# Performance work log

Hardware: AMD Instinct MI355X
Metric: run time of the kernel (lower is better)

## Reference

```python
import jax, jax.numpy as jnp
import numpy as np

B, T, NT, H, L, F, NH, R = 2, 1024, 30, 1024, 8, 2816, 16, 16
HD = H // NH
LORA_SCALE = 32.0 / 16.0  # lora_alpha / r
CLAMP = 10.0
EPS = 1e-6


def _rms(x, w):
    return x * jax.lax.rsqrt(jnp.mean(x * x, axis=-1, keepdims=True) + EPS) * w


def _rope(x):
    # x: [B,T,NH,HD] -- LLaMA rotary embedding
    half = HD // 2
    inv_freq = 1.0 / (10000.0 ** (jnp.arange(0, half, dtype=jnp.float32) / half))
    ang = jnp.arange(x.shape[1], dtype=jnp.float32)[:, None] * inv_freq  # [T,half]
    cos = jnp.concatenate([jnp.cos(ang), jnp.cos(ang)], -1)[None, :, None, :]
    sin = jnp.concatenate([jnp.sin(ang), jnp.sin(ang)], -1)[None, :, None, :]
    x1, x2 = x[..., :half], x[..., half:]
    return x * cos + jnp.concatenate([-x2, x1], -1) * sin


def _lora(x, W, A, Bm):
    # W: [in,out], A: [r,in], Bm: [out,r]  (dequantized base + LoRA update)
    return x @ W + ((x @ A.T) @ Bm.T) * LORA_SCALE


def setup_inputs():
    key = jax.random.key(0)
    ks = jax.random.split(key, 16)
    n = lambda k, s, sc=0.02: jax.random.normal(k, s, jnp.float32) * sc
    return {
        'x': jax.random.normal(ks[0], (B, T, NT), jnp.float32),
        'temperature': jnp.float32(1.0),
        'state_W': n(ks[1], (NT, H), 0.1),
        'state_b': jnp.zeros((H,), jnp.float32),
        'ln1': jnp.ones((L, H), jnp.float32),
        'ln2': jnp.ones((L, H), jnp.float32),
        'Wqkv': n(ks[2], (L, 3, H, H)),
        'Aqkv': n(ks[3], (L, 3, R, H)),
        'Bqkv': n(ks[4], (L, 3, H, R)),
        'Wo': n(ks[5], (L, H, H)),
        'Ao': n(ks[6], (L, R, H)),
        'Bo': n(ks[7], (L, H, R)),
        'Wgu': n(ks[8], (L, 2, H, F)),
        'Agu': n(ks[9], (L, 2, R, H)),
        'Bgu': n(ks[10], (L, 2, F, R)),
        'Wd': n(ks[11], (L, F, H)),
        'Ad': n(ks[12], (L, R, F)),
        'Bd': n(ks[13], (L, H, R)),
        'ln_f': jnp.ones((H,), jnp.float32),
        'head_W': n(ks[14], (H, NT + 1), 0.01),
        'head_b': jnp.zeros((NT + 1,), jnp.float32),
    }


def reference(x, temperature, state_W, state_b, ln1, ln2, Wqkv, Aqkv, Bqkv,
              Wo, Ao, Bo, Wgu, Agu, Bgu, Wd, Ad, Bd, ln_f, head_W, head_b):
    causal = jnp.tril(jnp.ones((T, T), bool))

    def layer(h, p):
        l1, l2, wqkv, aqkv, bqkv, wo, ao, bo, wgu, agu, bgu, wd, ad, bd = p
        hn = _rms(h, l1)
        qkv = jnp.einsum('bth,khd->kbtd', hn, wqkv)
        qkv = qkv + jnp.einsum('kbtr,kdr->kbtd',
                               jnp.einsum('bth,krh->kbtr', hn, aqkv), bqkv) * LORA_SCALE
        q = _rope(qkv[0].reshape(B, T, NH, HD))
        k = _rope(qkv[1].reshape(B, T, NH, HD))
        v = qkv[2].reshape(B, T, NH, HD)
        scores = jnp.einsum('bqhd,bkhd->bhqk', q, k) / np.sqrt(HD).astype(np.float32)
        scores = jnp.where(causal, scores, jnp.float32(-1e9))
        probs = jax.nn.softmax(scores, axis=-1)
        att = jnp.einsum('bhqk,bkhd->bqhd', probs, v).reshape(B, T, H)
        h = h + _lora(att, wo, ao, bo)
        hn2 = _rms(h, l2)
        gu = jnp.einsum('bth,khf->kbtf', hn2, wgu)
        gu = gu + jnp.einsum('kbtr,kfr->kbtf',
                             jnp.einsum('bth,krh->kbtr', hn2, agu), bgu) * LORA_SCALE
        act = jax.nn.silu(gu[0]) * gu[1]
        h = h + _lora(act, wd, ad, bd)
        return h, None

    h = x @ state_W + state_b  # state encoder -> inputs_embeds
    h, _ = jax.lax.scan(layer, h, (ln1, ln2, Wqkv, Aqkv, Bqkv, Wo, Ao, Bo,
                                   Wgu, Agu, Bgu, Wd, Ad, Bd))
    latent = _rms(h, ln_f)  # last hidden state
    logits = latent @ head_W + head_b
    logits_clamped = jnp.clip(logits, -CLAMP, CLAMP)
    portfolio_weights = jax.nn.softmax(logits_clamped / temperature, axis=-1)
    return portfolio_weights, logits_clamped
```

## Files before the change

### kernel.cpp

```cpp
#include <hip/hip_runtime.h>
#include <hip/hip_bf16.h>
#include <cstdint>

#define B_    2
#define T_    1024
#define NT_   30
#define H_    1024
#define L_    8
#define F_    2816
#define NH_   16
#define R_    16
#define HD_   64
#define M_    2048
#define NTP1_ 31

typedef unsigned short u16;
typedef short  s16x8 __attribute__((ext_vector_type(8)));
typedef unsigned short u16x4 __attribute__((ext_vector_type(4)));
typedef unsigned short u16x8 __attribute__((ext_vector_type(8)));
typedef float  f32x4 __attribute__((ext_vector_type(4)));

__device__ __forceinline__ u16 f2bf(float f){
  __hip_bfloat16 h = __float2bfloat16(f);
  return __builtin_bit_cast(unsigned short, h);
}
__device__ __forceinline__ float bf2f(u16 u){
  uint32_t v = (uint32_t)u << 16;
  return __builtin_bit_cast(float, v);
}

__device__ __forceinline__ void async16(const void* g, void* l){
  __builtin_amdgcn_global_load_lds((const __attribute__((address_space(1))) void*)g,
                                   (__attribute__((address_space(3))) void*)l, 16, 0, 0);
}

__global__ __launch_bounds__(256, 3) void fold_kernel(
    const float* __restrict__ W, const float* __restrict__ A,
    const float* __restrict__ Bm, u16* __restrict__ Wt,
    int K, int N, long strW, long strA, long strB, long strWt)
{
  const int mat = blockIdx.z;
  W  += (long)mat * strW;  A  += (long)mat * strA;
  Bm += (long)mat * strB;  Wt += (long)mat * strWt;
  const int k0 = blockIdx.x * 64, n0 = blockIdx.y * 64;
  __shared__ float Wt_s[64][65];
  __shared__ float As[16][64];
  __shared__ float Bs[64][20];
  const int tid = threadIdx.x;
  {
    const int kr = tid >> 4;
    const int n4 = (tid & 15) * 4;
    #pragma unroll
    for (int p = 0; p < 4; p++){
      int krow = p * 16 + kr;
      float4 w = *(const float4*)(W + (long)(k0 + krow) * N + n0 + n4);
      Wt_s[n4+0][krow] = w.x; Wt_s[n4+1][krow] = w.y;
      Wt_s[n4+2][krow] = w.z; Wt_s[n4+3][krow] = w.w;
    }
    const int r = tid >> 4, kc = (tid & 15) * 4;
    *(float4*)&As[r][kc] = *(const float4*)(A + (long)r * K + k0 + kc);
    const int nb = tid >> 2, r4 = (tid & 3) * 4;
    float4 b = *(const float4*)(Bm + (long)(n0 + nb) * 16 + r4);
    Bs[nb][r4+0]=b.x; Bs[nb][r4+1]=b.y; Bs[nb][r4+2]=b.z; Bs[nb][r4+3]=b.w;
  }
  __syncthreads();
  const int ko = (tid & 7) * 8;
  const int na = tid >> 3;
  float bq0[16], bq1[16];
  #pragma unroll
  for (int c = 0; c < 4; c++){
    *(float4*)&bq0[c*4] = *(const float4*)&Bs[na][c*4];
    *(float4*)&bq1[c*4] = *(const float4*)&Bs[na+32][c*4];
  }
  float l0[8] = {}, l1[8] = {};
  #pragma unroll
  for (int r = 0; r < 16; r++){
    float a[8];
    *(float4*)&a[0] = *(const float4*)&As[r][ko];
    *(float4*)&a[4] = *(const float4*)&As[r][ko+4];
    #pragma unroll
    for (int j = 0; j < 8; j++){
      l0[j] += a[j] * bq0[r];
      l1[j] += a[j] * bq1[r];
    }
  }
  u16x8 o0, o1;
  #pragma unroll
  for (int j = 0; j < 8; j++){
    o0[j] = f2bf(Wt_s[na][ko+j]    + 2.0f * l0[j]);
    o1[j] = f2bf(Wt_s[na+32][ko+j] + 2.0f * l1[j]);
  }
  *(u16x8*)(Wt + (long)(n0+na)*K    + k0 + ko) = o0;
  *(u16x8*)(Wt + (long)(n0+na+32)*K + k0 + ko) = o1;
}

__global__ __launch_bounds__(256) void embed_kernel(
    const float* __restrict__ x, const float* __restrict__ sw,
    const float* __restrict__ sb, float* __restrict__ h)
{
  const int m = blockIdx.x;
  const float* xr = x + (long)m * NT_;
  for (int jj = threadIdx.x; jj < H_; jj += 256){
    float acc = sb[jj];
    #pragma unroll
    for (int i = 0; i < NT_; i++) acc += xr[i] * sw[i * H_ + jj];
    h[(long)m * H_ + jj] = acc;
  }
}

__global__ __launch_bounds__(256) void rms_kernel(
    float* __restrict__ hsrc, const float* __restrict__ p0, const float* __restrict__ p1,
    const float* __restrict__ w, u16* __restrict__ outp, int fuse)
{
  const int m = blockIdx.x, t = threadIdx.x;
  float4 v = ((const float4*)(hsrc + (long)m * H_))[t];
  if (fuse){
    const float4 a = ((const float4*)(p0 + (long)m * H_))[t];
    const float4 b = ((const float4*)(p1 + (long)m * H_))[t];
    v.x += a.x + b.x; v.y += a.y + b.y; v.z += a.z + b.z; v.w += a.w + b.w;
    ((float4*)(hsrc + (long)m * H_))[t] = v;
  }
  float ss = v.x*v.x + v.y*v.y + v.z*v.z + v.w*v.w;
  #pragma unroll
  for (int off = 32; off >= 1; off >>= 1) ss += __shfl_xor(ss, off);
  __shared__ float red[4];
  if ((t & 63) == 0) red[t >> 6] = ss;
  __syncthreads();
  const float scale = rsqrtf((red[0]+red[1]+red[2]+red[3]) * (1.0f/H_) + 1e-6f);
  const float4 wv = ((const float4*)w)[t];
  u16x4 o;
  o[0] = f2bf(v.x*scale*wv.x); o[1] = f2bf(v.y*scale*wv.y);
  o[2] = f2bf(v.z*scale*wv.z); o[3] = f2bf(v.w*scale*wv.w);
  *(u16x4*)(outp + (long)m * H_ + t * 4) = o;
}

template<int OUTBF>
__global__ __launch_bounds__(256, 2) void gemm_bt(
    const u16* __restrict__ Ag, const u16* __restrict__ Btg, void* __restrict__ Cptr,
    int Ndim, int Klen, int Kstride, long zsA, long zsB, long zsC)
{
  Ag  += (long)blockIdx.z * zsA;
  Btg += (long)blockIdx.z * zsB;
  const int m0 = blockIdx.x * 128, n0 = blockIdx.y * 128;
  __shared__ alignas(16) u16 As[128 * 64];
  __shared__ alignas(16) u16 Bs[128 * 64];
  const int tid = threadIdx.x;
  const int wave = tid >> 6, lane = tid & 63;
  const int wm = (wave & 1) * 64, wn = (wave >> 1) * 64;
  const int fr = lane & 15, quad = lane >> 4;

  f32x4 acc[4][4] = {};

  for (int kt = 0; kt < Klen; kt += 64){
    __syncthreads();
    #pragma unroll
    for (int c = 0; c < 4; c++){
      int lin = c * 256 + tid;
      int row = lin >> 3, p = lin & 7;
      int gc = ((p ^ (row & 7)) * 8);
      async16(Ag  + (long)(m0 + row) * Kstride + kt + gc, As + lin * 8);
      async16(Btg + (long)(n0 + row) * Kstride + kt + gc, Bs + lin * 8);
    }
    __syncthreads();
    #pragma unroll
    for (int kk = 0; kk < 2; kk++){
      s16x8 af[4], bg[4];
      #pragma unroll
      for (int i = 0; i < 4; i++){
        int rA = wm + i * 16 + fr;
        af[i] = *(const s16x8*)(As + rA * 64 + (((kk*4 + quad) ^ (rA & 7)) * 8));
        int rB = wn + i * 16 + fr;
        bg[i] = *(const s16x8*)(Bs + rB * 64 + (((kk*4 + quad) ^ (rB & 7)) * 8));
      }
      #pragma unroll
      for (int i = 0; i < 4; i++)
        #pragma unroll
        for (int j = 0; j < 4; j++)
          acc[i][j] = __builtin_amdgcn_mfma_f32_16x16x32_bf16(af[i], bg[j], acc[i][j], 0, 0, 0);
    }
  }
  #pragma unroll
  for (int i = 0; i < 4; i++){
    int row0 = m0 + wm + i * 16 + quad * 4;
    #pragma unroll
    for (int j = 0; j < 4; j++){
      int col = n0 + wn + j * 16 + fr;
      #pragma unroll
      for (int r = 0; r < 4; r++){
        long idx = (long)(row0 + r) * Ndim + col;
        if (OUTBF){
          u16* C = (u16*)Cptr + (long)blockIdx.z * zsC;
          C[idx] = f2bf(acc[i][j][r]);
        } else {
          float* C = (float*)Cptr + (long)blockIdx.z * zsC;
          C[idx] = acc[i][j][r];
        }
      }
    }
  }
}

__global__ __launch_bounds__(256, 2) void gemm_gu(
    const u16* __restrict__ Ag, const u16* __restrict__ Bgw,
    const u16* __restrict__ Buw, u16* __restrict__ actb)
{
  const int m0 = blockIdx.x * 128, n0 = blockIdx.y * 128;
  __shared__ alignas(16) u16 As[128 * 64];
  __shared__ alignas(16) u16 Bg_[128 * 64];
  __shared__ alignas(16) u16 Bu_[128 * 64];
  const int tid = threadIdx.x;
  const int wave = tid >> 6, lane = tid & 63;
  const int wm = (wave & 1) * 64, wn = (wave >> 1) * 64;
  const int fr = lane & 15, quad = lane >> 4;

  f32x4 accg[4][4] = {}, accu[4][4] = {};

  for (int kt = 0; kt < H_; kt += 64){
    __syncthreads();
    #pragma unroll
    for (int c = 0; c < 4; c++){
      int lin = c * 256 + tid;
      int row = lin >> 3, p = lin & 7;
      int gc = ((p ^ (row & 7)) * 8);
      async16(Ag  + (long)(m0 + row) * H_ + kt + gc, As  + lin * 8);
      async16(Bgw + (long)(n0 + row) * H_ + kt + gc, Bg_ + lin * 8);
      async16(Buw + (long)(n0 + row) * H_ + kt + gc, Bu_ + lin * 8);
    }
    __syncthreads();
    #pragma unroll
    for (int kk = 0; kk < 2; kk++){
      s16x8 af[4], bb[4];
      #pragma unroll
      for (int i = 0; i < 4; i++){
        int rA = wm + i * 16 + fr;
        af[i] = *(const s16x8*)(As + rA * 64 + (((kk*4 + quad) ^ (rA & 7)) * 8));
      }
      #pragma unroll
      for (int i = 0; i < 4; i++){
        int rB = wn + i * 16 + fr;
        bb[i] = *(const s16x8*)(Bg_ + rB * 64 + (((kk*4 + quad) ^ (rB & 7)) * 8));
      }
      #pragma unroll
      for (int i = 0; i < 4; i++)
        #pragma unroll
        for (int j = 0; j < 4; j++)
          accg[i][j] = __builtin_amdgcn_mfma_f32_16x16x32_bf16(af[i], bb[j], accg[i][j], 0, 0, 0);
      #pragma unroll
      for (int i = 0; i < 4; i++){
        int rB = wn + i * 16 + fr;
        bb[i] = *(const s16x8*)(Bu_ + rB * 64 + (((kk*4 + quad) ^ (rB & 7)) * 8));
      }
      #pragma unroll
      for (int i = 0; i < 4; i++)
        #pragma unroll
        for (int j = 0; j < 4; j++)
          accu[i][j] = __builtin_amdgcn_mfma_f32_16x16x32_bf16(af[i], bb[j], accu[i][j], 0, 0, 0);
    }
  }
  #pragma unroll
  for (int i = 0; i < 4; i++){
    int row0 = m0 + wm + i * 16 + quad * 4;
    #pragma unroll
    for (int j = 0; j < 4; j++){
      int col = n0 + wn + j * 16 + fr;
      #pragma unroll
      for (int r = 0; r < 4; r++){
        float g = accg[i][j][r], u = accu[i][j][r];
        float act = g / (1.0f + __expf(-g)) * u;
        actb[(long)(row0 + r) * F_ + col] = f2bf(act);
      }
    }
  }
}

__global__ __launch_bounds__(256) void rope_kernel(
    const u16* __restrict__ qkv, u16* __restrict__ qr, u16* __restrict__ kr)
{
  const int m = blockIdx.x;
  const int b = m >> 10, t = m & 1023;
  for (int w = threadIdx.x; w < 1024; w += 256){
    const int sel = w >> 9;
    const int hh  = (w >> 5) & 15;
    const int i   = w & 31;
    const u16* src = qkv + (long)sel * M_ * H_ + (long)m * H_ + hh * HD_;
    float x1 = bf2f(src[i]), x2 = bf2f(src[i + 32]);
    float freq = exp2f((float)i * (-13.287712379549449f / 32.0f));
    float ang = (float)t * freq;
    float sn, cs; __sincosf(ang, &sn, &cs);
    u16* dst = (sel ? kr : qr) + ((long)((b * NH_ + hh) * T_ + t)) * HD_;
    dst[i]      = f2bf(x1 * cs - x2 * sn);
    dst[i + 32] = f2bf(x2 * cs + x1 * sn);
  }
}

__global__ __launch_bounds__(256) void vtrans_kernel(
    const u16* __restrict__ qkv, u16* __restrict__ vt)
{
  const int bh = blockIdx.x, b = bh >> 4, hh = bh & 15;
  const int d = threadIdx.x & 63, tc = threadIdx.x >> 6;
  const int t0 = blockIdx.y * 32 + tc * 8;
  const u16* src = qkv + (long)2 * M_ * H_ + (long)b * T_ * H_ + hh * HD_ + d;
  u16x8 o;
  #pragma unroll
  for (int j = 0; j < 8; j++) o[j] = src[(long)(t0 + j) * H_];
  *(u16x8*)(vt + ((long)bh * HD_ + d) * T_ + t0) = o;
}

__global__ __launch_bounds__(256, 2) void attn_kernel(
    const u16* __restrict__ qr, const u16* __restrict__ kr,
    const u16* __restrict__ vt, u16* __restrict__ att)
{
  const int qt = blockIdx.x;
  const int bh = blockIdx.y;
  const int b = bh >> 4, hh = bh & 15;
  __shared__ alignas(16) u16 Qs[64 * 64];
  __shared__ alignas(16) u16 Ks[128 * 64];
  __shared__ alignas(16) u16 Vs[64 * 128];
  __shared__ alignas(16) u16 Ps[64 * 136];
  const int tid = threadIdx.x;
  const int wave = tid >> 6, lane = tid & 63, fr = lane & 15, quad = lane >> 4;
  const int wrow = wave * 16;

  const u16* qg = qr + ((long)bh * T_ + qt * 64) * HD_;
  #pragma unroll
  for (int c = 0; c < 2; c++){
    int lin = c * 256 + tid, row = lin >> 3, p = lin & 7;
    async16(qg + row * HD_ + ((p ^ (row & 7)) * 8), Qs + lin * 8);
  }
  f32x4 o_acc[4] = {};
  float m_r[4] = {-1e30f, -1e30f, -1e30f, -1e30f};
  float l_r[4] = {};
  const u16* kgb = kr + (long)bh * T_ * HD_;
  const u16* vgb = vt + (long)bh * HD_ * T_;
  const int kmax = (qt * 64 + 63) >> 7;

  for (int kt = 0; kt <= kmax; kt++){
    __syncthreads();
    const u16* kg = kgb + (long)kt * 128 * HD_;
    #pragma unroll
    for (int c = 0; c < 4; c++){
      int lin = c * 256 + tid, row = lin >> 3, p = lin & 7;
      async16(kg + row * HD_ + ((p ^ (row & 7)) * 8), Ks + lin * 8);
    }
    #pragma unroll
    for (int c = 0; c < 4; c++){
      int lin = c * 256 + tid, row = lin >> 4, p = lin & 15;
      async16(vgb + (long)row * T_ + kt * 128 + ((p ^ (row & 15)) * 8), Vs + lin * 8);
    }
    __syncthreads();

    f32x4 s[8] = {};
    s16x8 aq[2];
    {
      int rA = wrow + fr;
      #pragma unroll
      for (int kk = 0; kk < 2; kk++)
        aq[kk] = *(const s16x8*)(Qs + rA * 64 + (((kk*4 + quad) ^ (rA & 7)) * 8));
    }
    #pragma unroll
    for (int ik = 0; ik < 8; ik++){
      #pragma unroll
      for (int kk = 0; kk < 2; kk++){
        int rB = ik * 16 + fr;
        s16x8 bk = *(const s16x8*)(Ks + rB * 64 + (((kk*4 + quad) ^ (rB & 7)) * 8));
        s[ik] = __builtin_amdgcn_mfma_f32_16x16x32_bf16(aq[kk], bk, s[ik], 0, 0, 0);
      }
    }
    const bool diag = (kt == kmax);
    #pragma unroll
    for (int r = 0; r < 4; r++){
      const int qgi = qt * 64 + wrow + quad * 4 + r;
      float tmax = -1e30f;
      #pragma unroll
      for (int ik = 0; ik < 8; ik++){
        float v = s[ik][r] * 0.125f;
        if (diag && (kt * 128 + ik * 16 + fr) > qgi) v = -1e9f;
        s[ik][r] = v;
        tmax = fmaxf(tmax, v);
      }
      #pragma unroll
      for (int off = 8; off >= 1; off >>= 1) tmax = fmaxf(tmax, __shfl_xor(tmax, off));
      const float mnew = fmaxf(m_r[r], tmax);
      const float alpha = __expf(m_r[r] - mnew);
      m_r[r] = mnew;
      float ts = 0.0f;
      const int prow = wrow + quad * 4 + r;
      #pragma unroll
      for (int ik = 0; ik < 8; ik++){
        float p = __expf(s[ik][r] - mnew);
        ts += p;
        Ps[prow * 136 + ik * 16 + fr] = f2bf(p);
      }
      #pragma unroll
      for (int off = 8; off >= 1; off >>= 1) ts += __shfl_xor(ts, off);
      l_r[r] = l_r[r] * alpha + ts;
      #pragma unroll
      for (int jd = 0; jd < 4; jd++) o_acc[jd][r] *= alpha;
    }
    #pragma unroll
    for (int kk2 = 0; kk2 < 4; kk2++){
      s16x8 ap = *(const s16x8*)(Ps + (wrow + fr) * 136 + kk2 * 32 + quad * 8);
      #pragma unroll
      for (int jd = 0; jd < 4; jd++){
        int rV = jd * 16 + fr;
        s16x8 bv = *(const s16x8*)(Vs + rV * 128 + (((kk2*4 + quad) ^ (rV & 15)) * 8));
        o_acc[jd] = __builtin_amdgcn_mfma_f32_16x16x32_bf16(ap, bv, o_acc[jd], 0, 0, 0);
      }
    }
  }
  #pragma unroll
  for (int r = 0; r < 4; r++){
    const int t_loc = qt * 64 + wrow + quad * 4 + r;
    const long rowbase = ((long)b * T_ + t_loc) * H_ + hh * HD_;
    const float inv = 1.0f / l_r[r];
    #pragma unroll
    for (int jd = 0; jd < 4; jd++)
      att[rowbase + jd * 16 + fr] = f2bf(o_acc[jd][r] * inv);
  }
}

__global__ __launch_bounds__(256) void head_kernel(
    const float* __restrict__ hsrc, const float* __restrict__ p0, const float* __restrict__ p1,
    const float* __restrict__ lnf, const float* __restrict__ hw, const float* __restrict__ hb,
    const float* __restrict__ temp, float* __restrict__ outp)
{
  const int m = blockIdx.x, t = threadIdx.x;
  __shared__ float lat[H_];
  __shared__ float red[4];
  __shared__ float part[8][32];
  float4 v = ((const float4*)(hsrc + (long)m * H_))[t];
  {
    const float4 a = ((const float4*)(p0 + (long)m * H_))[t];
    const float4 b = ((const float4*)(p1 + (long)m * H_))[t];
    v.x += a.x + b.x; v.y += a.y + b.y; v.z += a.z + b.z; v.w += a.w + b.w;
  }
  float ss = v.x*v.x + v.y*v.y + v.z*v.z + v.w*v.w;
  #pragma unroll
  for (int off = 32; off >= 1; off >>= 1) ss += __shfl_xor(ss, off);
  if ((t & 63) == 0) red[t >> 6] = ss;
  __syncthreads();
  const float scale = rsqrtf((red[0]+red[1]+red[2]+red[3]) * (1.0f/H_) + 1e-6f);
  const float4 wv = ((const float4*)lnf)[t];
  lat[t*4+0] = v.x*scale*wv.x;  lat[t*4+1] = v.y*scale*wv.y;
  lat[t*4+2] = v.z*scale*wv.z;  lat[t*4+3] = v.w*scale*wv.w;
  __syncthreads();
  const int j = t & 31, seg = t >> 5;
  float p = 0.0f;
  if (j < 31){
    const float* wp = hw + j;
    for (int k = seg * 128; k < seg * 128 + 128; k++) p += lat[k] * wp[(long)k * 31];
  }
  part[seg][j] = p;
  __syncthreads();
  if (t < 32){
    float dot = 0.0f;
    #pragma unroll
    for (int s2 = 0; s2 < 8; s2++) dot += part[s2][t];
    const float logit = (t < 31) ? dot + hb[t] : -1e30f;
    const float lc = fminf(fmaxf(logit, -10.0f), 10.0f);
    const float z = (t < 31) ? lc / temp[0] : -1e30f;
    float mx = z;
    #pragma unroll
    for (int off = 16; off >= 1; off >>= 1) mx = fmaxf(mx, __shfl_xor(mx, off, 32));
    const float e = (t < 31) ? __expf(z - mx) : 0.0f;
    float sum = e;
    #pragma unroll
    for (int off = 16; off >= 1; off >>= 1) sum += __shfl_xor(sum, off, 32);
    if (t < 31){
      outp[(long)m * NTP1_ + t] = e / sum;
      outp[(long)M_ * NTP1_ + (long)m * NTP1_ + t] = lc;
    }
  }
}

extern "C" void kernel_launch(void* const* d_in, const int* in_sizes, int n_in,
                              void* d_out, int out_size, void* d_ws, size_t ws_size,
                              hipStream_t stream) {
  const float* x    = (const float*)d_in[0];
  const float* temp = (const float*)d_in[1];
  const float* sW   = (const float*)d_in[2];
  const float* sb   = (const float*)d_in[3];
  const float* ln1  = (const float*)d_in[4];
  const float* ln2  = (const float*)d_in[5];
  const float* Wqkv = (const float*)d_in[6];
  const float* Aqkv = (const float*)d_in[7];
  const float* Bqkv = (const float*)d_in[8];
  const float* Wo   = (const float*)d_in[9];
  const float* Ao   = (const float*)d_in[10];
  const float* Bo   = (const float*)d_in[11];
  const float* Wgu  = (const float*)d_in[12];
  const float* Agu  = (const float*)d_in[13];
  const float* Bgu  = (const float*)d_in[14];
  const float* Wd   = (const float*)d_in[15];
  const float* Ad   = (const float*)d_in[16];
  const float* Bd   = (const float*)d_in[17];
  const float* lnf  = (const float*)d_in[18];
  const float* hW   = (const float*)d_in[19];
  const float* hb   = (const float*)d_in[20];
  float* out = (float*)d_out;

  uint8_t* ws = (uint8_t*)d_ws;
  size_t off = 0;
  auto alloc = [&](size_t bytes) -> void* {
    void* p = ws + off;
    off += (bytes + 255) & ~(size_t)255;
    return p;
  };
  u16*   wt_qkv = (u16*)  alloc((size_t)L_ * 3 * H_ * H_ * 2);
  u16*   wt_o   = (u16*)  alloc((size_t)L_ * H_ * H_ * 2);
  u16*   wt_gu  = (u16*)  alloc((size_t)L_ * 2 * F_ * H_ * 2);
  u16*   wt_d   = (u16*)  alloc((size_t)L_ * H_ * F_ * 2);
  float* h      = (float*)alloc((size_t)M_ * H_ * 4);
  u16*   hn     = (u16*)  alloc((size_t)M_ * H_ * 2);
  u16*   qkvb   = (u16*)  alloc((size_t)3 * M_ * H_ * 2);
  float* p0     = (float*)alloc((size_t)2 * M_ * H_ * 4);
  float* p1     = p0 + (size_t)M_ * H_;
  u16*   qr     = (u16*)  alloc((size_t)M_ * H_ * 2);
  u16*   krr    = (u16*)  alloc((size_t)M_ * H_ * 2);
  u16*   vtb    = (u16*)  alloc((size_t)M_ * H_ * 2);
  u16*   attb   = (u16*)  alloc((size_t)M_ * H_ * 2);
  u16*   actb   = (u16*)  alloc((size_t)M_ * F_ * 2);

  fold_kernel<<<dim3(16, 16, L_ * 3), 256, 0, stream>>>(Wqkv, Aqkv, Bqkv, wt_qkv,
      H_, H_, (long)H_ * H_, (long)R_ * H_, (long)H_ * R_, (long)H_ * H_);
  fold_kernel<<<dim3(16, 16, L_), 256, 0, stream>>>(Wo, Ao, Bo, wt_o,
      H_, H_, (long)H_ * H_, (long)R_ * H_, (long)H_ * R_, (long)H_ * H_);
  fold_kernel<<<dim3(16, 44, L_ * 2), 256, 0, stream>>>(Wgu, Agu, Bgu, wt_gu,
      H_, F_, (long)H_ * F_, (long)R_ * H_, (long)F_ * R_, (long)F_ * H_);
  fold_kernel<<<dim3(44, 16, L_), 256, 0, stream>>>(Wd, Ad, Bd, wt_d,
      F_, H_, (long)F_ * H_, (long)R_ * F_, (long)H_ * R_, (long)H_ * F_);

  embed_kernel<<<M_, 256, 0, stream>>>(x, sW, sb, h);

  for (int l = 0; l < L_; l++){
    rms_kernel<<<M_, 256, 0, stream>>>(h, p0, p1, ln1 + (long)l * H_, hn, l > 0 ? 1 : 0);
    gemm_bt<1><<<dim3(16, 8, 3), 256, 0, stream>>>(hn, wt_qkv + (long)l * 3 * H_ * H_,
        qkvb, H_, H_, H_, 0, (long)H_ * H_, (long)M_ * H_);
    rope_kernel<<<M_, 256, 0, stream>>>(qkvb, qr, krr);
    vtrans_kernel<<<dim3(B_ * NH_, T_ / 32), 256, 0, stream>>>(qkvb, vtb);
    attn_kernel<<<dim3(T_ / 64, B_ * NH_), 256, 0, stream>>>(qr, krr, vtb, attb);
    gemm_bt<0><<<dim3(16, 8, 2), 256, 0, stream>>>(attb, wt_o + (long)l * H_ * H_,
        p0, H_, 512, H_, 512, 512, (long)M_ * H_);
    rms_kernel<<<M_, 256, 0, stream>>>(h, p0, p1, ln2 + (long)l * H_, hn, 1);
    gemm_gu<<<dim3(16, 22), 256, 0, stream>>>(hn,
        wt_gu + (long)l * 2 * F_ * H_, wt_gu + (long)l * 2 * F_ * H_ + (long)F_ * H_, actb);
    gemm_bt<0><<<dim3(16, 8, 2), 256, 0, stream>>>(actb, wt_d + (long)l * H_ * F_,
        p0, H_, 1408, F_, 1408, 1408, (long)M_ * H_);
  }

  head_kernel<<<M_, 256, 0, stream>>>(h, p0, p1, lnf, hW, hb, temp, out);
}
```

Baseline: 1.728 ms.

## Double-buffer GEMM K-loop, widen split-K to four, fuse rope and V transpose

Both GEMM kernels move from a single 64-wide K tile to double-buffered 32-wide K tiles, so the async loads for the next step are issued before the MFMAs on the current step. This drops one barrier per iteration and lets the loads overlap with compute. Split-K for the output and down projections goes from 2 to 4 slices, giving more blocks per launch, and the residual/RMS and head kernels now sum four partial buffers. The rope and V-transpose kernels are merged into one launch, and gemm_bt asks for 3 blocks per CU through launch bounds. The cost is extra partial-sum memory traffic, and register pressure may rise at the higher occupancy target.

```diff
diff --git a/kernel.cpp b/kernel.cpp
--- a/kernel.cpp
+++ b/kernel.cpp
@@ -109,15 +109,17 @@
 }
 
 __global__ __launch_bounds__(256) void rms_kernel(
-    float* __restrict__ hsrc, const float* __restrict__ p0, const float* __restrict__ p1,
+    float* __restrict__ hsrc, const float* __restrict__ p,
     const float* __restrict__ w, u16* __restrict__ outp, int fuse)
 {
   const int m = blockIdx.x, t = threadIdx.x;
   float4 v = ((const float4*)(hsrc + (long)m * H_))[t];
   if (fuse){
-    const float4 a = ((const float4*)(p0 + (long)m * H_))[t];
-    const float4 b = ((const float4*)(p1 + (long)m * H_))[t];
-    v.x += a.x + b.x; v.y += a.y + b.y; v.z += a.z + b.z; v.w += a.w + b.w;
+    #pragma unroll
+    for (int z = 0; z < 4; z++){
+      const float4 a = ((const float4*)(p + (long)z * M_ * H_ + (long)m * H_))[t];
+      v.x += a.x; v.y += a.y; v.z += a.z; v.w += a.w;
+    }
     ((float4*)(hsrc + (long)m * H_))[t] = v;
   }
   float ss = v.x*v.x + v.y*v.y + v.z*v.z + v.w*v.w;
@@ -135,50 +137,59 @@
 }
 
 template<int OUTBF>
-__global__ __launch_bounds__(256, 2) void gemm_bt(
+__global__ __launch_bounds__(256, 3) void gemm_bt(
     const u16* __restrict__ Ag, const u16* __restrict__ Btg, void* __restrict__ Cptr,
     int Ndim, int Klen, int Kstride, long zsA, long zsB, long zsC)
 {
   Ag  += (long)blockIdx.z * zsA;
   Btg += (long)blockIdx.z * zsB;
   const int m0 = blockIdx.x * 128, n0 = blockIdx.y * 128;
-  __shared__ alignas(16) u16 As[128 * 64];
-  __shared__ alignas(16) u16 Bs[128 * 64];
+  __shared__ alignas(16) u16 As[2][128 * 32];
+  __shared__ alignas(16) u16 Bs[2][128 * 32];
   const int tid = threadIdx.x;
   const int wave = tid >> 6, lane = tid & 63;
   const int wm = (wave & 1) * 64, wn = (wave >> 1) * 64;
   const int fr = lane & 15, quad = lane >> 4;
 
+  const int r0 = tid >> 2, p0c = tid & 3;
+  const int r1 = (256 + tid) >> 2, p1c = tid & 3;
+  const int gc0 = (p0c ^ ((r0 >> 1) & 3)) * 8;
+  const int gc1 = (p1c ^ ((r1 >> 1) & 3)) * 8;
+
   f32x4 acc[4][4] = {};
-
-  for (int kt = 0; kt < Klen; kt += 64){
+  const int nk = Klen >> 5;
+
+  async16(Ag  + (long)(m0 + r0) * Kstride + gc0, &As[0][tid * 8]);
+  async16(Ag  + (long)(m0 + r1) * Kstride + gc1, &As[0][(256 + tid) * 8]);
+  async16(Btg + (long)(n0 + r0) * Kstride + gc0, &Bs[0][tid * 8]);
+  async16(Btg + (long)(n0 + r1) * Kstride + gc1, &Bs[0][(256 + tid) * 8]);
+  __syncthreads();
+
+  for (int k = 0; k < nk; k++){
+    const int cur = k & 1, nxt = cur ^ 1;
+    if (k + 1 < nk){
+      const int kt = (k + 1) << 5;
+      async16(Ag  + (long)(m0 + r0) * Kstride + kt + gc0, &As[nxt][tid * 8]);
+      async16(Ag  + (long)(m0 + r1) * Kstride + kt + gc1, &As[nxt][(256 + tid) * 8]);
+      async16(Btg + (long)(n0 + r0) * Kstride + kt + gc0, &Bs[nxt][tid * 8]);
+      async16(Btg + (long)(n0 + r1) * Kstride + kt + gc1, &Bs[nxt][(256 + tid) * 8]);
+    }
+    s16x8 af[4], bg[4];
+    #pragma unroll
+    for (int i = 0; i < 4; i++){
+      int rA = wm + i * 16 + fr;
+      af[i] = *(const s16x8*)(&As[cur][rA * 32 + ((quad ^ ((rA >> 1) & 3)) * 8)]);
+      int rB = wn + i * 16 + fr;
+      bg[i] = *(const s16x8*)(&Bs[cur][rB * 32 + ((quad ^ ((rB >> 1) & 3)) * 8)]);
+    }
+    #pragma unroll
+    for (int i = 0; i < 4; i++)
+      #pragma unroll
+      for (int j = 0; j < 4; j++)
+        acc[i][j] = __builtin_amdgcn_mfma_f32_16x16x32_bf16(af[i], bg[j], acc[i][j], 0, 0, 0);
     __syncthreads();
-    #pragma unroll
-    for (int c = 0; c < 4; c++){
-      int lin = c * 256 + tid;
-      int row = lin >> 3, p = lin & 7;
-      int gc = ((p ^ (row & 7)) * 8);
-      async16(Ag  + (long)(m0 + row) * Kstride + kt + gc, As + lin * 8);
-      async16(Btg + (long)(n0 + row) * Kstride + kt + gc, Bs + lin * 8);
-    }
-    __syncthreads();
-    #pragma unroll
-    for (int kk = 0; kk < 2; kk++){
-      s16x8 af[4], bg[4];
-      #pragma unroll
-      for (int i = 0; i < 4; i++){
-        int rA = wm + i * 16 + fr;
-        af[i] = *(const s16x8*)(As + rA * 64 + (((kk*4 + quad) ^ (rA & 7)) * 8));
-        int rB = wn + i * 16 + fr;
-        bg[i] = *(const s16x8*)(Bs + rB * 64 + (((kk*4 + quad) ^ (rB & 7)) * 8));
-      }
-      #pragma unroll
-      for (int i = 0; i < 4; i++)
-        #pragma unroll
-        for (int j = 0; j < 4; j++)
-          acc[i][j] = __builtin_amdgcn_mfma_f32_16x16x32_bf16(af[i], bg[j], acc[i][j], 0, 0, 0);
-    }
-  }
+  }
+
   #pragma unroll
   for (int i = 0; i < 4; i++){
     int row0 = m0 + wm + i * 16 + quad * 4;
@@ -205,58 +216,70 @@
     const u16* __restrict__ Buw, u16* __restrict__ actb)
 {
   const int m0 = blockIdx.x * 128, n0 = blockIdx.y * 128;
-  __shared__ alignas(16) u16 As[128 * 64];
-  __shared__ alignas(16) u16 Bg_[128 * 64];
-  __shared__ alignas(16) u16 Bu_[128 * 64];
+  __shared__ alignas(16) u16 As[2][128 * 32];
+  __shared__ alignas(16) u16 Bg_[2][128 * 32];
+  __shared__ alignas(16) u16 Bu_[2][128 * 32];
   const int tid = threadIdx.x;
   const int wave = tid >> 6, lane = tid & 63;
   const int wm = (wave & 1) * 64, wn = (wave >> 1) * 64;
   const int fr = lane & 15, quad = lane >> 4;
 
+  const int r0 = tid >> 2, p0c = tid & 3;
+  const int r1 = (256 + tid) >> 2, p1c = tid & 3;
+  const int gc0 = (p0c ^ ((r0 >> 1) & 3)) * 8;
+  const int gc1 = (p1c ^ ((r1 >> 1) & 3)) * 8;
+
   f32x4 accg[4][4] = {}, accu[4][4] = {};
-
-  for (int kt = 0; kt < H_; kt += 64){
+  const int nk = H_ >> 5;
+
+  async16(Ag  + (long)(m0 + r0) * H_ + gc0, &As[0][tid * 8]);
+  async16(Ag  + (long)(m0 + r1) * H_ + gc1, &As[0][(256 + tid) * 8]);
+  async16(Bgw + (long)(n0 + r0) * H_ + gc0, &Bg_[0][tid * 8]);
+  async16(Bgw + (long)(n0 + r1) * H_ + gc1, &Bg_[0][(256 + tid) * 8]);
+  async16(Buw + (long)(n0 + r0) * H_ + gc0, &Bu_[0][tid * 8]);
+  async16(Buw + (long)(n0 + r1) * H_ + gc1, &Bu_[0][(256 + tid) * 8]);
+  __syncthreads();
+
+  for (int k = 0; k < nk; k++){
+    const int cur = k & 1, nxt = cur ^ 1;
+    if (k + 1 < nk){
+      const int kt = (k + 1) << 5;
+      async16(Ag  + (long)(m0 + r0) * H_ + kt + gc0, &As[nxt][tid * 8]);
+      async16(Ag  + (long)(m0 + r1) * H_ + kt + gc1, &As[nxt][(256 + tid) * 8]);
+      async16(Bgw + (long)(n0 + r0) * H_ + kt + gc0, &Bg_[nxt][tid * 8]);
+      async16(Bgw + (long)(n0 + r1) * H_ + kt + gc1, &Bg_[nxt][(256 + tid) * 8]);
+      async16(Buw + (long)(n0 + r0) * H_ + kt + gc0, &Bu_[nxt][tid * 8]);
+      async16(Buw + (long)(n0 + r1) * H_ + kt + gc1, &Bu_[nxt][(256 + tid) * 8]);
+    }
+    s16x8 af[4], bb[4];
+    #pragma unroll
+    for (int i = 0; i < 4; i++){
+      int rA = wm + i * 16 + fr;
+      af[i] = *(const s16x8*)(&As[cur][rA * 32 + ((quad ^ ((rA >> 1) & 3)) * 8)]);
+    }
+    #pragma unroll
+    for (int i = 0; i < 4; i++){
+      int rB = wn + i * 16 + fr;
+      bb[i] = *(const s16x8*)(&Bg_[cur][rB * 32 + ((quad ^ ((rB >> 1) & 3)) * 8)]);
+    }
+    #pragma unroll
+    for (int i = 0; i < 4; i++)
+      #pragma unroll
+      for (int j = 0; j < 4; j++)
+        accg[i][j] = __builtin_amdgcn_mfma_f32_16x16x32_bf16(af[i], bb[j], accg[i][j], 0, 0, 0);
+    #pragma unroll
+    for (int i = 0; i < 4; i++){
+      int rB = wn + i * 16 + fr;
+      bb[i] = *(const s16x8*)(&Bu_[cur][rB * 32 + ((quad ^ ((rB >> 1) & 3)) * 8)]);
+    }
+    #pragma unroll
+    for (int i = 0; i < 4; i++)
+      #pragma unroll
+      for (int j = 0; j < 4; j++)
+        accu[i][j] = __builtin_amdgcn_mfma_f32_16x16x32_bf16(af[i], bb[j], accu[i][j], 0, 0, 0);
     __syncthreads();
-    #pragma unroll
-    for (int c = 0; c < 4; c++){
-      int lin = c * 256 + tid;
-      int row = lin >> 3, p = lin & 7;
-      int gc = ((p ^ (row & 7)) * 8);
-      async16(Ag  + (long)(m0 + row) * H_ + kt + gc, As  + lin * 8);
-      async16(Bgw + (long)(n0 + row) * H_ + kt + gc, Bg_ + lin * 8);
-      async16(Buw + (long)(n0 + row) * H_ + kt + gc, Bu_ + lin * 8);
-    }
-    __syncthreads();
-    #pragma unroll
-    for (int kk = 0; kk < 2; kk++){
-      s16x8 af[4], bb[4];
-      #pragma unroll
-      for (int i = 0; i < 4; i++){
-        int rA = wm + i * 16 + fr;
-        af[i] = *(const s16x8*)(As + rA * 64 + (((kk*4 + quad) ^ (rA & 7)) * 8));
-      }
-      #pragma unroll
-      for (int i = 0; i < 4; i++){
-        int rB = wn + i * 16 + fr;
-        bb[i] = *(const s16x8*)(Bg_ + rB * 64 + (((kk*4 + quad) ^ (rB & 7)) * 8));
-      }
-      #pragma unroll
-      for (int i = 0; i < 4; i++)
-        #pragma unroll
-        for (int j = 0; j < 4; j++)
-          accg[i][j] = __builtin_amdgcn_mfma_f32_16x16x32_bf16(af[i], bb[j], accg[i][j], 0, 0, 0);
-      #pragma unroll
-      for (int i = 0; i < 4; i++){
-        int rB = wn + i * 16 + fr;
-        bb[i] = *(const s16x8*)(Bu_ + rB * 64 + (((kk*4 + quad) ^ (rB & 7)) * 8));
-      }
-      #pragma unroll
-      for (int i = 0; i < 4; i++)
-        #pragma unroll
-        for (int j = 0; j < 4; j++)
-          accu[i][j] = __builtin_amdgcn_mfma_f32_16x16x32_bf16(af[i], bb[j], accu[i][j], 0, 0, 0);
-    }
-  }
+  }
+
   #pragma unroll
   for (int i = 0; i < 4; i++){
     int row0 = m0 + wm + i * 16 + quad * 4;
@@ -273,37 +296,39 @@
   }
 }
 
-__global__ __launch_bounds__(256) void rope_kernel(
-    const u16* __restrict__ qkv, u16* __restrict__ qr, u16* __restrict__ kr)
-{
-  const int m = blockIdx.x;
-  const int b = m >> 10, t = m & 1023;
-  for (int w = threadIdx.x; w < 1024; w += 256){
-    const int sel = w >> 9;
-    const int hh  = (w >> 5) & 15;
-    const int i   = w & 31;
-    const u16* src = qkv + (long)sel * M_ * H_ + (long)m * H_ + hh * HD_;
-    float x1 = bf2f(src[i]), x2 = bf2f(src[i + 32]);
-    float freq = exp2f((float)i * (-13.287712379549449f / 32.0f));
-    float ang = (float)t * freq;
-    float sn, cs; __sincosf(ang, &sn, &cs);
-    u16* dst = (sel ? kr : qr) + ((long)((b * NH_ + hh) * T_ + t)) * HD_;
-    dst[i]      = f2bf(x1 * cs - x2 * sn);
-    dst[i + 32] = f2bf(x2 * cs + x1 * sn);
-  }
-}
-
-__global__ __launch_bounds__(256) void vtrans_kernel(
-    const u16* __restrict__ qkv, u16* __restrict__ vt)
-{
-  const int bh = blockIdx.x, b = bh >> 4, hh = bh & 15;
-  const int d = threadIdx.x & 63, tc = threadIdx.x >> 6;
-  const int t0 = blockIdx.y * 32 + tc * 8;
-  const u16* src = qkv + (long)2 * M_ * H_ + (long)b * T_ * H_ + hh * HD_ + d;
-  u16x8 o;
-  #pragma unroll
-  for (int j = 0; j < 8; j++) o[j] = src[(long)(t0 + j) * H_];
-  *(u16x8*)(vt + ((long)bh * HD_ + d) * T_ + t0) = o;
+__global__ __launch_bounds__(256) void rope_vt_kernel(
+    const u16* __restrict__ qkv, u16* __restrict__ qr, u16* __restrict__ kr,
+    u16* __restrict__ vt)
+{
+  const int bid = blockIdx.x;
+  if (bid < M_){
+    const int m = bid;
+    const int b = m >> 10, t = m & 1023;
+    for (int w = threadIdx.x; w < 1024; w += 256){
+      const int sel = w >> 9;
+      const int hh  = (w >> 5) & 15;
+      const int i   = w & 31;
+      const u16* src = qkv + (long)sel * M_ * H_ + (long)m * H_ + hh * HD_;
+      float x1 = bf2f(src[i]), x2 = bf2f(src[i + 32]);
+      float freq = exp2f((float)i * (-13.287712379549449f / 32.0f));
+      float ang = (float)t * freq;
+      float sn, cs; __sincosf(ang, &sn, &cs);
+      u16* dst = (sel ? kr : qr) + ((long)((b * NH_ + hh) * T_ + t)) * HD_;
+      dst[i]      = f2bf(x1 * cs - x2 * sn);
+      dst[i + 32] = f2bf(x2 * cs + x1 * sn);
+    }
+  } else {
+    const int v = bid - M_;
+    const int bh = v >> 5, tch = v & 31;
+    const int b = bh >> 4, hh = bh & 15;
+    const int d = threadIdx.x & 63, tc = threadIdx.x >> 6;
+    const int t0 = tch * 32 + tc * 8;
+    const u16* src = qkv + (long)2 * M_ * H_ + (long)b * T_ * H_ + hh * HD_ + d;
+    u16x8 o;
+    #pragma unroll
+    for (int j = 0; j < 8; j++) o[j] = src[(long)(t0 + j) * H_];
+    *(u16x8*)(vt + ((long)bh * HD_ + d) * T_ + t0) = o;
+  }
 }
 
 __global__ __launch_bounds__(256, 2) void attn_kernel(
@@ -420,7 +445,7 @@
 }
 
 __global__ __launch_bounds__(256) void head_kernel(
-    const float* __restrict__ hsrc, const float* __restrict__ p0, const float* __restrict__ p1,
+    const float* __restrict__ hsrc, const float* __restrict__ p,
     const float* __restrict__ lnf, const float* __restrict__ hw, const float* __restrict__ hb,
     const float* __restrict__ temp, float* __restrict__ outp)
 {
@@ -429,10 +454,10 @@
   __shared__ float red[4];
   __shared__ float part[8][32];
   float4 v = ((const float4*)(hsrc + (long)m * H_))[t];
-  {
-    const float4 a = ((const float4*)(p0 + (long)m * H_))[t];
-    const float4 b = ((const float4*)(p1 + (long)m * H_))[t];
-    v.x += a.x + b.x; v.y += a.y + b.y; v.z += a.z + b.z; v.w += a.w + b.w;
+  #pragma unroll
+  for (int z = 0; z < 4; z++){
+    const float4 a = ((const float4*)(p + (long)z * M_ * H_ + (long)m * H_))[t];
+    v.x += a.x; v.y += a.y; v.z += a.z; v.w += a.w;
   }
   float ss = v.x*v.x + v.y*v.y + v.z*v.z + v.w*v.w;
   #pragma unroll
@@ -445,12 +470,12 @@
   lat[t*4+2] = v.z*scale*wv.z;  lat[t*4+3] = v.w*scale*wv.w;
   __syncthreads();
   const int j = t & 31, seg = t >> 5;
-  float p = 0.0f;
+  float pp = 0.0f;
   if (j < 31){
     const float* wp = hw + j;
-    for (int k = seg * 128; k < seg * 128 + 128; k++) p += lat[k] * wp[(long)k * 31];
-  }
-  part[seg][j] = p;
+    for (int k = seg * 128; k < seg * 128 + 128; k++) pp += lat[k] * wp[(long)k * 31];
+  }
+  part[seg][j] = pp;
   __syncthreads();
   if (t < 32){
     float dot = 0.0f;
@@ -513,8 +538,7 @@
   float* h      = (float*)alloc((size_t)M_ * H_ * 4);
   u16*   hn     = (u16*)  alloc((size_t)M_ * H_ * 2);
   u16*   qkvb   = (u16*)  alloc((size_t)3 * M_ * H_ * 2);
-  float* p0     = (float*)alloc((size_t)2 * M_ * H_ * 4);
-  float* p1     = p0 + (size_t)M_ * H_;
+  float* p      = (float*)alloc((size_t)4 * M_ * H_ * 4);
   u16*   qr     = (u16*)  alloc((size_t)M_ * H_ * 2);
   u16*   krr    = (u16*)  alloc((size_t)M_ * H_ * 2);
   u16*   vtb    = (u16*)  alloc((size_t)M_ * H_ * 2);
@@ -533,20 +557,19 @@
   embed_kernel<<<M_, 256, 0, stream>>>(x, sW, sb, h);
 
   for (int l = 0; l < L_; l++){
-    rms_kernel<<<M_, 256, 0, stream>>>(h, p0, p1, ln1 + (long)l * H_, hn, l > 0 ? 1 : 0);
+    rms_kernel<<<M_, 256, 0, stream>>>(h, p, ln1 + (long)l * H_, hn, l > 0 ? 1 : 0);
     gemm_bt<1><<<dim3(16, 8, 3), 256, 0, stream>>>(hn, wt_qkv + (long)l * 3 * H_ * H_,
         qkvb, H_, H_, H_, 0, (long)H_ * H_, (long)M_ * H_);
-    rope_kernel<<<M_, 256, 0, stream>>>(qkvb, qr, krr);
-    vtrans_kernel<<<dim3(B_ * NH_, T_ / 32), 256, 0, stream>>>(qkvb, vtb);
+    rope_vt_kernel<<<M_ + 1024, 256, 0, stream>>>(qkvb, qr, krr, vtb);
     attn_kernel<<<dim3(T_ / 64, B_ * NH_), 256, 0, stream>>>(qr, krr, vtb, attb);
-    gemm_bt<0><<<dim3(16, 8, 2), 256, 0, stream>>>(attb, wt_o + (long)l * H_ * H_,
-        p0, H_, 512, H_, 512, 512, (long)M_ * H_);
-    rms_kernel<<<M_, 256, 0, stream>>>(h, p0, p1, ln2 + (long)l * H_, hn, 1);
+    gemm_bt<0><<<dim3(16, 8, 4), 256, 0, stream>>>(attb, wt_o + (long)l * H_ * H_,
+        p, H_, 256, H_, 256, 256, (long)M_ * H_);
+    rms_kernel<<<M_, 256, 0, stream>>>(h, p, ln2 + (long)l * H_, hn, 1);
     gemm_gu<<<dim3(16, 22), 256, 0, stream>>>(hn,
         wt_gu + (long)l * 2 * F_ * H_, wt_gu + (long)l * 2 * F_ * H_ + (long)F_ * H_, actb);
-    gemm_bt<0><<<dim3(16, 8, 2), 256, 0, stream>>>(actb, wt_d + (long)l * H_ * F_,
-        p0, H_, 1408, F_, 1408, 1408, (long)M_ * H_);
-  }
-
-  head_kernel<<<M_, 256, 0, stream>>>(h, p0, p1, lnf, hW, hb, temp, out);
-}
+    gemm_bt<0><<<dim3(16, 8, 4), 256, 0, stream>>>(actb, wt_d + (long)l * H_ * F_,
+        p, H_, 704, F_, 704, 704, (long)M_ * H_);
+  }
+
+  head_kernel<<<M_, 256, 0, stream>>>(h, p, lnf, hW, hb, temp, out);
+}
```

After: 1.877 ms. 8.6% more time.
